# Kernel tuning notes

Hardware: AMD Instinct MI355X
Metric: run time of the kernel (lower is better)

The kernel has to match this reference:

```python
import jax, jax.numpy as jnp
import numpy as np
from jax import lax

C = 64
K = 9
PAD = 4  # torch uses padding=4 with kernel 9 -> same-size output


def conv1d(x, w, b):
    """x: [B, C, N], w: [O, I, K], b: [O] -> [B, O, N]."""
    y = lax.conv_general_dilated(
        x, w, window_strides=(1,), padding=[(PAD, PAD)],
        dimension_numbers=("NCH", "OIH", "NCH"))
    return y + b[None, :, None]


def directional_scan(seq, w, b):
    """seq: [L, B, C, N]. seq[i] += relu(conv(seq[i-1])) sequentially (i=1..L-1)."""
    first = seq[0]

    def step(carry, row):
        new = row + jax.nn.relu(conv1d(carry, w, b))
        return new, new

    _, rest = lax.scan(step, first, seq[1:])
    return jnp.concatenate([first[None], rest], axis=0)


def scnn_forward(x, w_ud, b_ud, w_du, b_du, w_lr, b_lr, w_rl, b_rl):
    # up -> down (scan over height, conv along width)
    seq = jnp.transpose(x, (2, 0, 1, 3))            # [H, B, C, W]
    seq = directional_scan(seq, w_ud, b_ud)
    # down -> up (reverse height)
    seq = directional_scan(seq[::-1], w_du, b_du)[::-1]
    x = jnp.transpose(seq, (1, 2, 0, 3))            # [B, C, H, W]
    # left -> right (scan over width, conv along height)
    seq = jnp.transpose(x, (3, 0, 1, 2))            # [W, B, C, H]
    seq = directional_scan(seq, w_lr, b_lr)
    # right -> left (reverse width)
    seq = directional_scan(seq[::-1], w_rl, b_rl)[::-1]
    return jnp.transpose(seq, (1, 2, 3, 0))         # [B, C, H, W]


def setup_inputs() -> dict:
    key = jax.random.key(0)
    ks = jax.random.split(key, 9)
    B, H, W = 8, 256, 512
    fan_in = C * K
    scale = 1.0 / np.sqrt(fan_in)
    x = jax.random.normal(ks[0], (B, C, H, W), dtype=jnp.float32)
    w_ud = jax.random.uniform(ks[1], (C, C, K), jnp.float32, -scale, scale)
    b_ud = jax.random.uniform(ks[2], (C,), jnp.float32, -scale, scale)
    w_du = jax.random.uniform(ks[3], (C, C, K), jnp.float32, -scale, scale)
    b_du = jax.random.uniform(ks[4], (C,), jnp.float32, -scale, scale)
    w_lr = jax.random.uniform(ks[5], (C, C, K), jnp.float32, -scale, scale)
    b_lr = jax.random.uniform(ks[6], (C,), jnp.float32, -scale, scale)
    w_rl = jax.random.uniform(ks[7], (C, C, K), jnp.float32, -scale, scale)
    b_rl = jax.random.uniform(ks[8], (C,), jnp.float32, -scale, scale)
    return {"x": x, "w_ud": w_ud, "b_ud": b_ud, "w_du": w_du, "b_du": b_du,
            "w_lr": w_lr, "b_lr": b_lr, "w_rl": w_rl, "b_rl": b_rl}


def reference(x, w_ud, b_ud, w_du, b_du, w_lr, b_lr, w_rl, b_rl):
    return scnn_forward(x, w_ud, b_ud, w_du, b_du, w_lr, b_lr, w_rl, b_rl)
```

## Files before the change

### kernel.cpp

```cpp
#include <hip/hip_runtime.h>

static constexpr int B_ = 8;
static constexpr int C_ = 64;
static constexpr int H_ = 256;
static constexpr int W_ = 512;
static constexpr int K_ = 9;
static constexpr int PAD_ = 4;

static constexpr int T_ = 16;
static constexpr int WIN_ = 24;
static constexpr int CIW_ = 72;
static constexpr int NB_ = 8;

typedef unsigned long long u64;
typedef unsigned int u32;
typedef __attribute__((ext_vector_type(8))) short bf16x8;
typedef __attribute__((ext_vector_type(4))) float f32x4;

static constexpr size_t XCC_OFF = 0;
static constexpr size_t XCC_PER_DIR = 256 * 4;
static constexpr size_t TAG_OFF = 64ull << 10;
static constexpr size_t TAG_PER_DIR = 128ull << 10;
static constexpr size_t HALO_A_OFF = 1ull << 20;
static constexpr size_t HALO_A_PER_DIR = 2ull << 20;
static constexpr size_t INIT_BYTES = HALO_A_OFF + 4 * HALO_A_PER_DIR;
static constexpr size_t HALO_P_OFF = 9ull << 20;
static constexpr size_t HALO_P_PER_DIR = 1ull << 20;
static constexpr size_t TBUF_OFF = 16ull << 20;

__device__ __forceinline__ void l2_put_u64(u64* p, u64 v) {
    asm volatile("global_atomic_swap_x2 %0, %1, off" :: "v"(p), "v"(v)
                 : "memory");
}
__device__ __forceinline__ u64 l2_get_u64(const u64* p) {
    u64 v;
    asm volatile("global_atomic_add_x2 %0, %1, %2, off sc0\n\t"
                 "s_waitcnt vmcnt(0)"
                 : "=&v"(v) : "v"(p), "v"(0ull) : "memory");
    return v;
}
__device__ __forceinline__ u64 ic_get_u64(const u64* p) {
    return __hip_atomic_load(p, __ATOMIC_RELAXED, __HIP_MEMORY_SCOPE_AGENT);
}
__device__ __forceinline__ void ic_put_u64(u64* p, u64 v) {
    (void)__hip_atomic_exchange(p, v, __ATOMIC_RELAXED,
                                __HIP_MEMORY_SCOPE_AGENT);
}
__device__ __forceinline__ u64 pack_tag(float val, unsigned tag) {
    return (u64)__float_as_uint(val) | ((u64)tag << 32);
}
__device__ __forceinline__ u64 pack2f(float a, float b) {
    return (u64)__float_as_uint(a) | ((u64)__float_as_uint(b) << 32);
}
__device__ __forceinline__ unsigned xcc_id() {
    unsigned v;
    asm volatile("s_getreg_b32 %0, hwreg(HW_REG_XCC_ID)" : "=s"(v));
    return v & 0xffu;
}
__device__ __forceinline__ unsigned short f2bf(float f) {
    const u32 u = __float_as_uint(f);
    return (unsigned short)((u + 0x7fffu + ((u >> 16) & 1u)) >> 16);
}

__global__ __launch_bounds__(256, 1) void scan_mfma_kernel(
    float* __restrict__ buf, const float* __restrict__ w,
    const float* __restrict__ bias, const int N,
    const long long rowStride, const long long colStride,
    const long long chanStride, const int startRow, const int rowDir,
    const int numSteps, u64* __restrict__ halo_a, u64* __restrict__ halo_p,
    u64* __restrict__ tags, unsigned* __restrict__ xccmap)
{
    __shared__ __attribute__((aligned(16))) unsigned short prevT[WIN_][CIW_];
    __shared__ unsigned s_ic[2];

    const int tid = threadIdx.x;
    const int wv = tid >> 6;
    const int lane = tid & 63;
    const int n = lane & 15;
    const int q = lane >> 4;
    const int blk = blockIdx.x;
    const int b = blk & 7;
    const int tile = blk >> 3;
    const int TPB = N / T_;
    const int t0 = tile * T_;
    const bool hasL = tile > 0;
    const bool hasR = tile < TPB - 1;

    bool icL = hasL, icR = hasR;
    if (halo_a != nullptr) {
        if (tid == 0) {
            const unsigned my = xcc_id();
            __hip_atomic_store(xccmap + blk, 0x100u | my, __ATOMIC_RELAXED,
                               __HIP_MEMORY_SCOPE_AGENT);
            unsigned xl = 0, xr = 0;
            if (hasL)
                while (!((xl = __hip_atomic_load(xccmap + blk - NB_,
                                                 __ATOMIC_RELAXED,
                                                 __HIP_MEMORY_SCOPE_AGENT)) &
                         0x100u))
                    __builtin_amdgcn_s_sleep(1);
            if (hasR)
                while (!((xr = __hip_atomic_load(xccmap + blk + NB_,
                                                 __ATOMIC_RELAXED,
                                                 __HIP_MEMORY_SCOPE_AGENT)) &
                         0x100u))
                    __builtin_amdgcn_s_sleep(1);
            s_ic[0] = (hasL && ((xl & 0xffu) != my)) ? 1u : 0u;
            s_ic[1] = (hasR && ((xr & 0xffu) != my)) ? 1u : 0u;
        }
        __syncthreads();
        icL = s_ic[0] != 0;
        icR = s_ic[1] != 0;
    }

    const long long base = (long long)b * C_ * chanStride;

    bf16x8 af[18];
    {
        const float* wr = w + (long long)(wv * 16 + n) * (C_ * K_);
#pragma unroll
        for (int t = 0; t < 18; ++t) {
            const int tap = t >> 1;
            const int ci0 = (t & 1) * 32 + q * 8;
            bf16x8 a;
#pragma unroll
            for (int j = 0; j < 8; ++j)
                a[j] = (short)f2bf(wr[(ci0 + j) * K_ + tap]);
            af[t] = a;
        }
    }
    const int co0 = wv * 16 + q * 4;
    float bv[4];
#pragma unroll
    for (int i = 0; i < 4; ++i) bv[i] = bias[co0 + i];

    for (int s = 0; s < numSteps; ++s) {
        const int irow = startRow + s * rowDir;
        const long long orow = base + (long long)irow * rowStride;
        const int col = t0 + n;

        float xv[4];
#pragma unroll
        for (int i = 0; i < 4; ++i)
            xv[i] = buf[orow + (long long)(co0 + i) * chanStride +
                        (long long)col * colStride];

        if (s == 0) {
            const long long pr = base + (long long)(irow - rowDir) * rowStride;
            for (int idx = tid; idx < WIN_ * C_; idx += 256) {
                const int c = idx >> 6, ci = idx & 63;
                const int gc = t0 + c - PAD_;
                float v = 0.f;
                if (gc >= 0 && gc < N)
                    v = buf[pr + (long long)ci * chanStride +
                            (long long)gc * colStride];
                prevT[c][ci] = f2bf(v);
            }
        } else {
            const int par = (s - 1) & 1;
            const unsigned want = (unsigned)s;
            {
                const int side = wv >> 1;
                const bool hasS = side ? hasR : hasL;
                const bool icS = side ? icR : icL;
                if (hasS && !icS) {
                    const int nb = side ? (blk + NB_) : (blk - NB_);
                    const size_t slot =
                        (size_t)((nb * 2 + par) * 2 + (side ^ 1));
                    if (lane == 0) {
                        const u64* tp = tags + slot * 8;
                        while ((unsigned)l2_get_u64(tp) != want)
                            __builtin_amdgcn_s_sleep(1);
                    }
                    const int k = (wv & 1) * 64 + lane;
                    const u64 v = l2_get_u64(halo_p + slot * 128 + k);
                    const int hc = k >> 5;
                    const int cp = k & 31;
                    const int off = side ? (T_ + 4) : 0;
                    prevT[off + hc][2 * cp + 0] =
                        f2bf(__uint_as_float((u32)v));
                    prevT[off + hc][2 * cp + 1] =
                        f2bf(__uint_as_float((u32)(v >> 32)));
                }
            }
            if ((hasL && icL) || (hasR && icR)) {
                if (hasL && icL) {
                    const u64* p = halo_a +
                        (size_t)(((blk - NB_) * 2 + par) * 2 + 1) * 256 + tid;
                    u64 v = ic_get_u64(p);
                    while ((unsigned)(v >> 32) != want) {
                        __builtin_amdgcn_s_sleep(1);
                        v = ic_get_u64(p);
                    }
                    prevT[tid >> 6][tid & 63] =
                        f2bf(__uint_as_float((u32)v));
                }
                if (hasR && icR) {
                    const u64* p = halo_a +
                        (size_t)(((blk + NB_) * 2 + par) * 2 + 0) * 256 + tid;
                    u64 v = ic_get_u64(p);
                    while ((unsigned)(v >> 32) != want) {
                        __builtin_amdgcn_s_sleep(1);
                        v = ic_get_u64(p);
                    }
                    prevT[T_ + 4 + (tid >> 6)][tid & 63] =
                        f2bf(__uint_as_float((u32)v));
                }
            }
        }
        __syncthreads();

        f32x4 acc = {0.f, 0.f, 0.f, 0.f};
#pragma unroll
        for (int t = 0; t < 18; ++t) {
            const int tap = t >> 1;
            const int ci0 = (t & 1) * 32 + q * 8;
            const bf16x8 bf = *(const bf16x8*)&prevT[n + tap][ci0];
            acc = __builtin_amdgcn_mfma_f32_16x16x32_bf16(af[t], bf, acc,
                                                          0, 0, 0);
        }

        float r[4];
#pragma unroll
        for (int i = 0; i < 4; ++i)
            r[i] = xv[i] + fmaxf(acc[i] + bv[i], 0.f);

        const int epar = s & 1;
        if (s != numSteps - 1 && halo_a != nullptr) {
            const unsigned tag = (unsigned)(s + 1);
            const bool isL = (n < 4) && hasL;
            const bool isR = (n >= T_ - 4) && hasR;
            if (isL || isR) {
                const int side = isR ? 1 : 0;
                const int hc = isR ? (n - (T_ - 4)) : n;
                const bool ic = isR ? icR : icL;
                if (!ic) {
                    u64* p = halo_p +
                        (size_t)((blk * 2 + epar) * 2 + side) * 128 +
                        hc * 32 + (co0 >> 1);
                    l2_put_u64(p, pack2f(r[0], r[1]));
                    l2_put_u64(p + 1, pack2f(r[2], r[3]));
                } else {
                    u64* p = halo_a +
                        (size_t)((blk * 2 + epar) * 2 + side) * 256 +
                        hc * 64 + co0;
#pragma unroll
                    for (int i = 0; i < 4; ++i)
                        ic_put_u64(p + i, pack_tag(r[i], tag));
                }
            }
        }

        __syncthreads();

        if (s != numSteps - 1 && halo_a != nullptr) {
            if (tid == 0 && hasL && !icL)
                l2_put_u64(tags + (size_t)((blk * 2 + epar) * 2 + 0) * 8,
                           (u64)(s + 1));
            if (tid == 64 && hasR && !icR)
                l2_put_u64(tags + (size_t)((blk * 2 + epar) * 2 + 1) * 8,
                           (u64)(s + 1));
        }

#pragma unroll
        for (int i = 0; i < 4; ++i)
            buf[orow + (long long)(co0 + i) * chanStride +
                (long long)col * colStride] = r[i];

        const u64 pk = (u64)f2bf(r[0]) | ((u64)f2bf(r[1]) << 16) |
                       ((u64)f2bf(r[2]) << 32) | ((u64)f2bf(r[3]) << 48);
        *(u64*)&prevT[4 + n][co0] = pk;
    }
}

__global__ __launch_bounds__(256) void transpose_kernel(
    const float* __restrict__ in, float* __restrict__ out,
    const int R, const int S)
{
    __shared__ float tile[32][33];
    const size_t plane = (size_t)blockIdx.z * R * S;
    const int s0 = blockIdx.x * 32;
    const int r0 = blockIdx.y * 32;
    const int tx = threadIdx.x;
    const int ty = threadIdx.y;
#pragma unroll
    for (int j = 0; j < 32; j += 8)
        tile[ty + j][tx] = in[plane + (size_t)(r0 + ty + j) * S + s0 + tx];
    __syncthreads();
#pragma unroll
    for (int j = 0; j < 32; j += 8)
        out[plane + (size_t)(s0 + ty + j) * R + r0 + tx] = tile[tx][ty + j];
}

static void launch_dir(float* buf, const float* w, const float* bias, int N,
                       long long rowStride, long long colStride,
                       long long chanStride, int startRow, int rowDir,
                       int numSteps, u64* halo_a, u64* halo_p, u64* tags,
                       unsigned* xccmap, bool persistent, hipStream_t stream)
{
    const int nblocks = 8 * (N / T_);
    if (persistent) {
        scan_mfma_kernel<<<nblocks, 256, 0, stream>>>(
            buf, w, bias, N, rowStride, colStride, chanStride, startRow,
            rowDir, numSteps, halo_a, halo_p, tags, xccmap);
    } else {
        for (int s = 0; s < numSteps; ++s)
            scan_mfma_kernel<<<nblocks, 256, 0, stream>>>(
                buf, w, bias, N, rowStride, colStride, chanStride,
                startRow + s * rowDir, rowDir, 1, nullptr, nullptr, nullptr,
                nullptr);
    }
}

extern "C" void kernel_launch(void* const* d_in, const int* in_sizes, int n_in,
                              void* d_out, int out_size, void* d_ws,
                              size_t ws_size, hipStream_t stream)
{
    const float* x    = (const float*)d_in[0];
    const float* w_ud = (const float*)d_in[1];
    const float* b_ud = (const float*)d_in[2];
    const float* w_du = (const float*)d_in[3];
    const float* b_du = (const float*)d_in[4];
    const float* w_lr = (const float*)d_in[5];
    const float* b_lr = (const float*)d_in[6];
    const float* w_rl = (const float*)d_in[7];
    const float* b_rl = (const float*)d_in[8];
    float* out = (float*)d_out;

    const size_t total = (size_t)B_ * C_ * H_ * W_;
    const long long chan = (long long)H_ * W_;

    const bool haveSync = ws_size >= HALO_P_OFF + 4 * HALO_P_PER_DIR;
    const bool haveT = ws_size >= TBUF_OFF + total * sizeof(float);

    float* wsT = (float*)((char*)d_ws + TBUF_OFF);

    hipMemcpyAsync(out, x, total * sizeof(float), hipMemcpyDeviceToDevice,
                   stream);
    if (haveSync) hipMemsetAsync(d_ws, 0, INIT_BYTES, stream);

    u64* ha[4];
    u64* hp[4];
    u64* tg[4];
    unsigned* xm[4];
    for (int d = 0; d < 4; ++d) {
        ha[d] = (u64*)((char*)d_ws + HALO_A_OFF + d * HALO_A_PER_DIR);
        hp[d] = (u64*)((char*)d_ws + HALO_P_OFF + d * HALO_P_PER_DIR);
        tg[d] = (u64*)((char*)d_ws + TAG_OFF + d * TAG_PER_DIR);
        xm[d] = (unsigned*)((char*)d_ws + XCC_OFF + d * XCC_PER_DIR);
    }

    launch_dir(out, w_ud, b_ud, W_, (long long)W_, 1LL, chan,
               1, +1, H_ - 1, ha[0], hp[0], tg[0], xm[0], haveSync, stream);
    launch_dir(out, w_du, b_du, W_, (long long)W_, 1LL, chan,
               H_ - 2, -1, H_ - 1, ha[1], hp[1], tg[1], xm[1], haveSync,
               stream);

    if (haveT) {
        {
            dim3 gt(W_ / 32, H_ / 32, B_ * C_);
            transpose_kernel<<<gt, dim3(32, 8), 0, stream>>>(out, wsT, H_, W_);
        }
        launch_dir(wsT, w_lr, b_lr, H_, (long long)H_, 1LL, chan,
                   1, +1, W_ - 1, ha[2], hp[2], tg[2], xm[2], haveSync,
                   stream);
        launch_dir(wsT, w_rl, b_rl, H_, (long long)H_, 1LL, chan,
                   W_ - 2, -1, W_ - 1, ha[3], hp[3], tg[3], xm[3], haveSync,
                   stream);
        {
            dim3 gt(H_ / 32, W_ / 32, B_ * C_);
            transpose_kernel<<<gt, dim3(32, 8), 0, stream>>>(wsT, out, W_, H_);
        }
    } else {
        launch_dir(out, w_lr, b_lr, H_, 1LL, (long long)W_, chan,
                   1, +1, W_ - 1, ha[2], hp[2], tg[2], xm[2], haveSync,
                   stream);
        launch_dir(out, w_rl, b_rl, H_, 1LL, (long long)W_, chan,
                   W_ - 2, -1, W_ - 1, ha[3], hp[3], tg[3], xm[3], haveSync,
                   stream);
    }
}
```

Measured before the change: 3.113 ms.

## Use trapezoidal two-step halo exchange to halve inter-block synchronization

```diff
diff --git a/kernel.cpp b/kernel.cpp
--- a/kernel.cpp
+++ b/kernel.cpp
@@ -8,7 +8,7 @@
 static constexpr int PAD_ = 4;
 
 static constexpr int T_ = 16;
-static constexpr int WIN_ = 24;
+static constexpr int WC_ = 36;
 static constexpr int CIW_ = 72;
 static constexpr int NB_ = 8;
 
@@ -18,15 +18,11 @@
 typedef __attribute__((ext_vector_type(4))) float f32x4;
 
 static constexpr size_t XCC_OFF = 0;
-static constexpr size_t XCC_PER_DIR = 256 * 4;
 static constexpr size_t TAG_OFF = 64ull << 10;
-static constexpr size_t TAG_PER_DIR = 128ull << 10;
-static constexpr size_t HALO_A_OFF = 1ull << 20;
-static constexpr size_t HALO_A_PER_DIR = 2ull << 20;
-static constexpr size_t INIT_BYTES = HALO_A_OFF + 4 * HALO_A_PER_DIR;
-static constexpr size_t HALO_P_OFF = 9ull << 20;
-static constexpr size_t HALO_P_PER_DIR = 1ull << 20;
-static constexpr size_t TBUF_OFF = 16ull << 20;
+static constexpr size_t INIT_BYTES = 128ull << 10;
+static constexpr size_t HALO_OFF = 1ull << 20;
+static constexpr size_t SLOT_U64 = 192;
+static constexpr size_t TBUF_OFF = 4ull << 20;
 
 __device__ __forceinline__ void l2_put_u64(u64* p, u64 v) {
     asm volatile("global_atomic_swap_x2 %0, %1, off" :: "v"(p), "v"(v)
@@ -46,11 +42,12 @@
     (void)__hip_atomic_exchange(p, v, __ATOMIC_RELAXED,
                                 __HIP_MEMORY_SCOPE_AGENT);
 }
-__device__ __forceinline__ u64 pack_tag(float val, unsigned tag) {
-    return (u64)__float_as_uint(val) | ((u64)tag << 32);
-}
-__device__ __forceinline__ u64 pack2f(float a, float b) {
-    return (u64)__float_as_uint(a) | ((u64)__float_as_uint(b) << 32);
+__device__ __forceinline__ u64 halo_put(u64* p, u64 v, bool ic) {
+    if (ic) ic_put_u64(p, v); else l2_put_u64(p, v);
+    return 0;
+}
+__device__ __forceinline__ u64 halo_get(const u64* p, bool ic) {
+    return ic ? ic_get_u64(p) : l2_get_u64(p);
 }
 __device__ __forceinline__ unsigned xcc_id() {
     unsigned v;
@@ -61,16 +58,24 @@
     const u32 u = __float_as_uint(f);
     return (unsigned short)((u + 0x7fffu + ((u >> 16) & 1u)) >> 16);
 }
-
-__global__ __launch_bounds__(256, 1) void scan_mfma_kernel(
+__device__ __forceinline__ float bf2f(unsigned short h) {
+    return __uint_as_float((u32)h << 16);
+}
+__device__ __forceinline__ u64 pack4bf(const float* r) {
+    return (u64)f2bf(r[0]) | ((u64)f2bf(r[1]) << 16) |
+           ((u64)f2bf(r[2]) << 32) | ((u64)f2bf(r[3]) << 48);
+}
+
+__global__ __launch_bounds__(256, 1) void scan_trap_kernel(
     float* __restrict__ buf, const float* __restrict__ w,
     const float* __restrict__ bias, const int N,
     const long long rowStride, const long long colStride,
     const long long chanStride, const int startRow, const int rowDir,
-    const int numSteps, u64* __restrict__ halo_a, u64* __restrict__ halo_p,
-    u64* __restrict__ tags, unsigned* __restrict__ xccmap)
+    const int numSteps, u64* __restrict__ halo, u64* __restrict__ tags,
+    unsigned* __restrict__ xccmap, const u64 tagBase)
 {
-    __shared__ __attribute__((aligned(16))) unsigned short prevT[WIN_][CIW_];
+    __shared__ __attribute__((aligned(16))) unsigned short prevT[WC_][CIW_];
+    __shared__ __attribute__((aligned(8))) unsigned short xh[2][4][64];
     __shared__ unsigned s_ic[2];
 
     const int tid = threadIdx.x;
@@ -78,6 +83,8 @@
     const int lane = tid & 63;
     const int n = lane & 15;
     const int q = lane >> 4;
+    const int coq = wv * 4 + q;
+    const int co0 = coq * 4;
     const int blk = blockIdx.x;
     const int b = blk & 7;
     const int tile = blk >> 3;
@@ -85,9 +92,10 @@
     const int t0 = tile * T_;
     const bool hasL = tile > 0;
     const bool hasR = tile < TPB - 1;
+    const int ownc = (n >= 8) ? (t0 + n - 8) : (t0 + 8 + n);
 
     bool icL = hasL, icR = hasR;
-    if (halo_a != nullptr) {
+    if (halo != nullptr) {
         if (tid == 0) {
             const unsigned my = xcc_id();
             __hip_atomic_store(xccmap + blk, 0x100u | my, __ATOMIC_RELAXED,
@@ -129,147 +137,174 @@
             af[t] = a;
         }
     }
-    const int co0 = wv * 16 + q * 4;
     float bv[4];
 #pragma unroll
     for (int i = 0; i < 4; ++i) bv[i] = bias[co0 + i];
 
-    for (int s = 0; s < numSteps; ++s) {
-        const int irow = startRow + s * rowDir;
-        const long long orow = base + (long long)irow * rowStride;
-        const int col = t0 + n;
-
-        float xv[4];
-#pragma unroll
-        for (int i = 0; i < 4; ++i)
-            xv[i] = buf[orow + (long long)(co0 + i) * chanStride +
-                        (long long)col * colStride];
-
-        if (s == 0) {
-            const long long pr = base + (long long)(irow - rowDir) * rowStride;
-            for (int idx = tid; idx < WIN_ * C_; idx += 256) {
-                const int c = idx >> 6, ci = idx & 63;
-                const int gc = t0 + c - PAD_;
-                float v = 0.f;
-                if (gc >= 0 && gc < N)
-                    v = buf[pr + (long long)ci * chanStride +
-                            (long long)gc * colStride];
-                prevT[c][ci] = f2bf(v);
-            }
-        } else {
-            const int par = (s - 1) & 1;
-            const unsigned want = (unsigned)s;
+    {
+        const long long pr = base + (long long)(startRow - rowDir) * rowStride;
+        for (int idx = tid; idx < WC_ * C_; idx += 256) {
+            const int c = idx >> 6, ci = idx & 63;
+            const int gc = t0 - 12 + c;
+            float v = 0.f;
+            if (gc >= 0 && gc < N)
+                v = buf[pr + (long long)ci * chanStride +
+                        (long long)gc * colStride];
+            prevT[c][ci] = f2bf(v);
+        }
+        if (tid < 512) ((unsigned short*)xh)[tid] = 0;
+    }
+
+    float prevR[4] = {0.f, 0.f, 0.f, 0.f};
+
+    for (int s0 = 0; s0 < numSteps; s0 += 2) {
+        const int g = s0 >> 1;
+        const int d = (numSteps - s0 >= 2) ? 2 : 1;
+        const int par = g & 1;
+
+        if (halo != nullptr) {
+            const u64 tagv = tagBase + (u64)g + 1;
+            if (g > 0) {
+                const int side = (n >= 8) ? 0 : 1;
+                const bool has = side ? hasR : hasL;
+                if (has) {
+                    const bool ic = side ? icR : icL;
+                    const int c = (n >= 8) ? (n - 8) : n;
+                    u64* p = halo +
+                        (size_t)((blk * 2 + par) * 2 + side) * SLOT_U64 +
+                        c * 16 + coq;
+                    halo_put(p, pack4bf(prevR), ic);
+                }
+            }
+            if (d == 2 && tid < 128) {
+                const int side = tid >> 6, c = (tid >> 4) & 3, cq = tid & 15;
+                const bool has = side ? hasR : hasL;
+                if (has) {
+                    const bool ic = side ? icR : icL;
+                    const int col = t0 + (side ? 12 + c : c);
+                    const long long orow =
+                        base + (long long)(startRow + s0 * rowDir) * rowStride;
+                    float f[4];
+#pragma unroll
+                    for (int i = 0; i < 4; ++i)
+                        f[i] = buf[orow + (long long)(cq * 4 + i) * chanStride +
+                                   (long long)col * colStride];
+                    u64* p = halo +
+                        (size_t)((blk * 2 + par) * 2 + side) * SLOT_U64 +
+                        128 + c * 16 + cq;
+                    halo_put(p, pack4bf(f), ic);
+                }
+            }
+            __syncthreads();
+            if (tid == 0 && hasL)
+                halo_put(tags + (size_t)((blk * 2 + par) * 2 + 0) * 8, tagv,
+                         icL);
+            if (tid == 64 && hasR)
+                halo_put(tags + (size_t)((blk * 2 + par) * 2 + 1) * 8, tagv,
+                         icR);
+            if (tid == 0 && hasL) {
+                const u64* tp =
+                    tags + (size_t)(((blk - NB_) * 2 + par) * 2 + 1) * 8;
+                while (halo_get(tp, icL) < tagv) __builtin_amdgcn_s_sleep(1);
+            }
+            if (tid == 64 && hasR) {
+                const u64* tp =
+                    tags + (size_t)(((blk + NB_) * 2 + par) * 2 + 0) * 8;
+                while (halo_get(tp, icR) < tagv) __builtin_amdgcn_s_sleep(1);
+            }
+            __syncthreads();
+            if (g > 0) {
+                const int side = tid >> 7;
+                const int word = tid & 127, c = word >> 4, cq = word & 15;
+                const bool has = side ? hasR : hasL;
+                if (has) {
+                    const bool ic = side ? icR : icL;
+                    const int nb = side ? (blk + NB_) : (blk - NB_);
+                    const u64* p = halo +
+                        (size_t)((nb * 2 + par) * 2 + (side ^ 1)) * SLOT_U64 +
+                        word;
+                    const u64 v = halo_get(p, ic);
+                    const int rel = side ? (28 + c) : (4 + c);
+                    *(u64*)&prevT[rel][cq * 4] = v;
+                }
+            }
+            if (d == 2 && tid < 128) {
+                const int side = tid >> 6, c = (tid >> 4) & 3, cq = tid & 15;
+                const bool has = side ? hasR : hasL;
+                if (has) {
+                    const bool ic = side ? icR : icL;
+                    const int nb = side ? (blk + NB_) : (blk - NB_);
+                    const u64* p = halo +
+                        (size_t)((nb * 2 + par) * 2 + (side ^ 1)) * SLOT_U64 +
+                        128 + c * 16 + cq;
+                    *(u64*)&xh[side][c][cq * 4] = halo_get(p, ic);
+                }
+            }
+        }
+        __syncthreads();
+
+        for (int j = 0; j < d; ++j) {
+            const int row = startRow + (s0 + j) * rowDir;
+            const long long orow = base + (long long)row * rowStride;
+
+            float xo[4];
+#pragma unroll
+            for (int i = 0; i < 4; ++i)
+                xo[i] = buf[orow + (long long)(co0 + i) * chanStride +
+                            (long long)ownc * colStride];
+
+            f32x4 a0 = {0.f, 0.f, 0.f, 0.f};
+            f32x4 a1 = {0.f, 0.f, 0.f, 0.f};
+#pragma unroll
+            for (int t = 0; t < 18; ++t) {
+                const int tap = t >> 1;
+                const int ci0 = (t & 1) * 32 + q * 8;
+                const bf16x8 b0 = *(const bf16x8*)&prevT[n + tap][ci0];
+                const bf16x8 b1 = *(const bf16x8*)&prevT[16 + n + tap][ci0];
+                a0 = __builtin_amdgcn_mfma_f32_16x16x32_bf16(af[t], b0, a0,
+                                                             0, 0, 0);
+                a1 = __builtin_amdgcn_mfma_f32_16x16x32_bf16(af[t], b1, a1,
+                                                             0, 0, 0);
+            }
+
+            float xt0[4], xt1[4];
             {
-                const int side = wv >> 1;
-                const bool hasS = side ? hasR : hasL;
-                const bool icS = side ? icR : icL;
-                if (hasS && !icS) {
-                    const int nb = side ? (blk + NB_) : (blk - NB_);
-                    const size_t slot =
-                        (size_t)((nb * 2 + par) * 2 + (side ^ 1));
-                    if (lane == 0) {
-                        const u64* tp = tags + slot * 8;
-                        while ((unsigned)l2_get_u64(tp) != want)
-                            __builtin_amdgcn_s_sleep(1);
-                    }
-                    const int k = (wv & 1) * 64 + lane;
-                    const u64 v = l2_get_u64(halo_p + slot * 128 + k);
-                    const int hc = k >> 5;
-                    const int cp = k & 31;
-                    const int off = side ? (T_ + 4) : 0;
-                    prevT[off + hc][2 * cp + 0] =
-                        f2bf(__uint_as_float((u32)v));
-                    prevT[off + hc][2 * cp + 1] =
-                        f2bf(__uint_as_float((u32)(v >> 32)));
+                const u64 hvL = *(const u64*)&xh[0][(n - 4) & 3][co0];
+                const u64 hvR = *(const u64*)&xh[1][(n - 8) & 3][co0];
+#pragma unroll
+                for (int i = 0; i < 4; ++i) {
+                    xt0[i] = (n >= 8)
+                                 ? xo[i]
+                                 : bf2f((unsigned short)(hvL >> (16 * i)));
+                    xt1[i] = (n < 8)
+                                 ? xo[i]
+                                 : bf2f((unsigned short)(hvR >> (16 * i)));
                 }
             }
-            if ((hasL && icL) || (hasR && icR)) {
-                if (hasL && icL) {
-                    const u64* p = halo_a +
-                        (size_t)(((blk - NB_) * 2 + par) * 2 + 1) * 256 + tid;
-                    u64 v = ic_get_u64(p);
-                    while ((unsigned)(v >> 32) != want) {
-                        __builtin_amdgcn_s_sleep(1);
-                        v = ic_get_u64(p);
-                    }
-                    prevT[tid >> 6][tid & 63] =
-                        f2bf(__uint_as_float((u32)v));
-                }
-                if (hasR && icR) {
-                    const u64* p = halo_a +
-                        (size_t)(((blk + NB_) * 2 + par) * 2 + 0) * 256 + tid;
-                    u64 v = ic_get_u64(p);
-                    while ((unsigned)(v >> 32) != want) {
-                        __builtin_amdgcn_s_sleep(1);
-                        v = ic_get_u64(p);
-                    }
-                    prevT[T_ + 4 + (tid >> 6)][tid & 63] =
-                        f2bf(__uint_as_float((u32)v));
-                }
-            }
-        }
-        __syncthreads();
-
-        f32x4 acc = {0.f, 0.f, 0.f, 0.f};
-#pragma unroll
-        for (int t = 0; t < 18; ++t) {
-            const int tap = t >> 1;
-            const int ci0 = (t & 1) * 32 + q * 8;
-            const bf16x8 bf = *(const bf16x8*)&prevT[n + tap][ci0];
-            acc = __builtin_amdgcn_mfma_f32_16x16x32_bf16(af[t], bf, acc,
-                                                          0, 0, 0);
-        }
-
-        float r[4];
-#pragma unroll
-        for (int i = 0; i < 4; ++i)
-            r[i] = xv[i] + fmaxf(acc[i] + bv[i], 0.f);
-
-        const int epar = s & 1;
-        if (s != numSteps - 1 && halo_a != nullptr) {
-            const unsigned tag = (unsigned)(s + 1);
-            const bool isL = (n < 4) && hasL;
-            const bool isR = (n >= T_ - 4) && hasR;
-            if (isL || isR) {
-                const int side = isR ? 1 : 0;
-                const int hc = isR ? (n - (T_ - 4)) : n;
-                const bool ic = isR ? icR : icL;
-                if (!ic) {
-                    u64* p = halo_p +
-                        (size_t)((blk * 2 + epar) * 2 + side) * 128 +
-                        hc * 32 + (co0 >> 1);
-                    l2_put_u64(p, pack2f(r[0], r[1]));
-                    l2_put_u64(p + 1, pack2f(r[2], r[3]));
-                } else {
-                    u64* p = halo_a +
-                        (size_t)((blk * 2 + epar) * 2 + side) * 256 +
-                        hc * 64 + co0;
-#pragma unroll
-                    for (int i = 0; i < 4; ++i)
-                        ic_put_u64(p + i, pack_tag(r[i], tag));
-                }
-            }
-        }
-
-        __syncthreads();
-
-        if (s != numSteps - 1 && halo_a != nullptr) {
-            if (tid == 0 && hasL && !icL)
-                l2_put_u64(tags + (size_t)((blk * 2 + epar) * 2 + 0) * 8,
-                           (u64)(s + 1));
-            if (tid == 64 && hasR && !icR)
-                l2_put_u64(tags + (size_t)((blk * 2 + epar) * 2 + 1) * 8,
-                           (u64)(s + 1));
-        }
-
-#pragma unroll
-        for (int i = 0; i < 4; ++i)
-            buf[orow + (long long)(co0 + i) * chanStride +
-                (long long)col * colStride] = r[i];
-
-        const u64 pk = (u64)f2bf(r[0]) | ((u64)f2bf(r[1]) << 16) |
-                       ((u64)f2bf(r[2]) << 32) | ((u64)f2bf(r[3]) << 48);
-        *(u64*)&prevT[4 + n][co0] = pk;
+            float r0v[4], r1v[4];
+#pragma unroll
+            for (int i = 0; i < 4; ++i) {
+                r0v[i] = xt0[i] + fmaxf(a0[i] + bv[i], 0.f);
+                r1v[i] = xt1[i] + fmaxf(a1[i] + bv[i], 0.f);
+            }
+#pragma unroll
+            for (int i = 0; i < 4; ++i)
+                prevR[i] = (n >= 8) ? r0v[i] : r1v[i];
+
+            __syncthreads();
+
+            const int g0 = t0 - 8 + n;
+            if (g0 >= 0) *(u64*)&prevT[4 + n][co0] = pack4bf(r0v);
+            const int g1 = t0 + 8 + n;
+            if (g1 < N) *(u64*)&prevT[20 + n][co0] = pack4bf(r1v);
+
+#pragma unroll
+            for (int i = 0; i < 4; ++i)
+                buf[orow + (long long)(co0 + i) * chanStride +
+                    (long long)ownc * colStride] = prevR[i];
+
+            __syncthreads();
+        }
     }
 }
 
@@ -295,20 +330,20 @@
 static void launch_dir(float* buf, const float* w, const float* bias, int N,
                        long long rowStride, long long colStride,
                        long long chanStride, int startRow, int rowDir,
-                       int numSteps, u64* halo_a, u64* halo_p, u64* tags,
-                       unsigned* xccmap, bool persistent, hipStream_t stream)
+                       int numSteps, u64* halo, u64* tags, unsigned* xccmap,
+                       u64 tagBase, bool persistent, hipStream_t stream)
 {
     const int nblocks = 8 * (N / T_);
     if (persistent) {
-        scan_mfma_kernel<<<nblocks, 256, 0, stream>>>(
+        scan_trap_kernel<<<nblocks, 256, 0, stream>>>(
             buf, w, bias, N, rowStride, colStride, chanStride, startRow,
-            rowDir, numSteps, halo_a, halo_p, tags, xccmap);
+            rowDir, numSteps, halo, tags, xccmap, tagBase);
     } else {
         for (int s = 0; s < numSteps; ++s)
-            scan_mfma_kernel<<<nblocks, 256, 0, stream>>>(
+            scan_trap_kernel<<<nblocks, 256, 0, stream>>>(
                 buf, w, bias, N, rowStride, colStride, chanStride,
                 startRow + s * rowDir, rowDir, 1, nullptr, nullptr, nullptr,
-                nullptr);
+                0ull);
     }
 }
 
@@ -330,30 +365,26 @@
     const size_t total = (size_t)B_ * C_ * H_ * W_;
     const long long chan = (long long)H_ * W_;
 
-    const bool haveSync = ws_size >= HALO_P_OFF + 4 * HALO_P_PER_DIR;
+    const bool haveSync = ws_size >= TBUF_OFF;
     const bool haveT = ws_size >= TBUF_OFF + total * sizeof(float);
 
+    u64* halo = (u64*)((char*)d_ws + HALO_OFF);
+    u64* tags = (u64*)((char*)d_ws + TAG_OFF);
     float* wsT = (float*)((char*)d_ws + TBUF_OFF);
 
     hipMemcpyAsync(out, x, total * sizeof(float), hipMemcpyDeviceToDevice,
                    stream);
     if (haveSync) hipMemsetAsync(d_ws, 0, INIT_BYTES, stream);
 
-    u64* ha[4];
-    u64* hp[4];
-    u64* tg[4];
     unsigned* xm[4];
-    for (int d = 0; d < 4; ++d) {
-        ha[d] = (u64*)((char*)d_ws + HALO_A_OFF + d * HALO_A_PER_DIR);
-        hp[d] = (u64*)((char*)d_ws + HALO_P_OFF + d * HALO_P_PER_DIR);
-        tg[d] = (u64*)((char*)d_ws + TAG_OFF + d * TAG_PER_DIR);
-        xm[d] = (unsigned*)((char*)d_ws + XCC_OFF + d * XCC_PER_DIR);
-    }
+    for (int d = 0; d < 4; ++d)
+        xm[d] = (unsigned*)((char*)d_ws + XCC_OFF + d * 1024);
 
     launch_dir(out, w_ud, b_ud, W_, (long long)W_, 1LL, chan,
-               1, +1, H_ - 1, ha[0], hp[0], tg[0], xm[0], haveSync, stream);
+               1, +1, H_ - 1, halo, tags, xm[0], 0ull << 20, haveSync,
+               stream);
     launch_dir(out, w_du, b_du, W_, (long long)W_, 1LL, chan,
-               H_ - 2, -1, H_ - 1, ha[1], hp[1], tg[1], xm[1], haveSync,
+               H_ - 2, -1, H_ - 1, halo, tags, xm[1], 1ull << 20, haveSync,
                stream);
 
     if (haveT) {
@@ -362,21 +393,21 @@
             transpose_kernel<<<gt, dim3(32, 8), 0, stream>>>(out, wsT, H_, W_);
         }
         launch_dir(wsT, w_lr, b_lr, H_, (long long)H_, 1LL, chan,
-                   1, +1, W_ - 1, ha[2], hp[2], tg[2], xm[2], haveSync,
+                   1, +1, W_ - 1, halo, tags, xm[2], 2ull << 20, haveSync,
                    stream);
         launch_dir(wsT, w_rl, b_rl, H_, (long long)H_, 1LL, chan,
-                   W_ - 2, -1, W_ - 1, ha[3], hp[3], tg[3], xm[3], haveSync,
-                   stream);
+                   W_ - 2, -1, W_ - 1, halo, tags, xm[3], 3ull << 20,
+                   haveSync, stream);
         {
             dim3 gt(H_ / 32, W_ / 32, B_ * C_);
             transpose_kernel<<<gt, dim3(32, 8), 0, stream>>>(wsT, out, W_, H_);
         }
     } else {
         launch_dir(out, w_lr, b_lr, H_, 1LL, (long long)W_, chan,
-                   1, +1, W_ - 1, ha[2], hp[2], tg[2], xm[2], haveSync,
+                   1, +1, W_ - 1, halo, tags, xm[2], 2ull << 20, haveSync,
                    stream);
         launch_dir(out, w_rl, b_rl, H_, 1LL, (long long)W_, chan,
-                   W_ - 2, -1, W_ - 1, ha[3], hp[3], tg[3], xm[3], haveSync,
-                   stream);
-    }
-}
+                   W_ - 2, -1, W_ - 1, halo, tags, xm[3], 3ull << 20,
+                   haveSync, stream);
+    }
+}
```

After: 3.741 ms. 1.2x slower.
